# Optimization experiments

Measured on AMD Instinct MI355X. Metric: run time of the kernel, lower is better.

Reference implementation:

```python
import jax, jax.numpy as jnp
import numpy as np

B, S, D, E, H, K = 2, 2048, 1024, 8, 4096, 2


def setup_inputs() -> dict:
    key = jax.random.key(0)
    ks = jax.random.split(key, 8)
    w = lambda i, shape: jax.random.normal(ks[i], shape, jnp.float32) * 0.02
    return {
        "x": jax.random.normal(ks[0], (B, S, D), jnp.float32),
        "noise": jax.random.normal(ks[1], (B, S, E), jnp.float32),
        "Wg": w(2, (E, D)),
        "noise_weight": jnp.zeros((E,), jnp.float32),
        "W1": w(3, (E, D, H)),
        "b1": jnp.zeros((E, H), jnp.float32),
        "W2": w(4, (E, D, H)),
        "b2": jnp.zeros((E, H), jnp.float32),
        "Wp": w(5, (E, H, D)),
        "bp": jnp.zeros((E, D), jnp.float32),
        "k": K,
    }


def reference(x, noise, Wg, noise_weight, W1, b1, W2, b2, Wp, bp, k):
    Bb, Ss, Dd = x.shape
    Ee = Wg.shape[0]
    # --- noisy top-k gate (noisy_std = 1.0) ---
    logits = jnp.einsum('bsd,ed->bse', x, Wg)
    noisy = logits + noise * noise_weight            # [B,S,E]
    vals, idx = jax.lax.top_k(noisy, k)              # [B,S,k]
    oh = jax.nn.one_hot(idx, Ee, dtype=x.dtype)      # [B,S,k,E]
    sel = oh.sum(axis=-2) > 0                        # [B,S,E] selected mask
    scat = (oh * vals[..., None]).sum(axis=-2)       # scatter topk logits
    sparse = jnp.where(sel, scat, -jnp.inf)
    gate = jax.nn.softmax(sparse, axis=-1)           # zero weight off-topk
    # --- dense-equivalent expert compute (gate==0 off top-k => same math as masked dispatch) ---
    xf = x.reshape(Bb * Ss, Dd)                      # [T,D]
    gf = gate.reshape(Bb * Ss, Ee)                   # [T,E]
    h1 = jnp.einsum('td,edh->eth', xf, W1) + b1[:, None, :]
    h2 = jnp.einsum('td,edh->eth', xf, W2) + b2[:, None, :]
    hh = h1 * jax.nn.silu(h2)                        # SwiGLU
    outs = jnp.einsum('eth,ehd->etd', hh, Wp) + bp[:, None, :]
    final = jnp.einsum('etd,te->td', outs, gf).reshape(Bb, Ss, Dd)
    return final, idx
```

## Files before the change

kernel.cpp:

```cpp
#include <hip/hip_runtime.h>
#include <math.h>

#define Bc 2
#define Sc 2048
#define Dc 1024
#define Ec 8
#define Hc 4096
#define Tc (Bc*Sc)
#define NSLOT (Tc*2)
#define FINAL_N ((size_t)Tc*Dc)
#define BK 32

typedef float f32x4 __attribute__((ext_vector_type(4)));
typedef __bf16 bf16x8 __attribute__((ext_vector_type(8)));

__device__ __forceinline__ unsigned short f2bf(float f) {
    union { float f; unsigned int u; } v; v.f = f;
    return (unsigned short)((v.u + 0x7fffu + ((v.u >> 16) & 1u)) >> 16);
}

__device__ __forceinline__ void gload16(const unsigned short* g, unsigned short* l) {
    __builtin_amdgcn_global_load_lds(
        (const __attribute__((address_space(1))) unsigned int*)g,
        (__attribute__((address_space(3))) unsigned int*)l,
        16, 0, 0);
}

__device__ __forceinline__ void fence_bar() {
    __builtin_amdgcn_sched_barrier(0);
    asm volatile("s_barrier" ::: "memory");
    __builtin_amdgcn_sched_barrier(0);
}

__global__ void k_cvt_x(const float* __restrict__ x, unsigned short* __restrict__ xbf) {
    int gid = blockIdx.x * 256 + threadIdx.x;
    const float4* p = (const float4*)x + (size_t)gid * 2;
    float4 a = p[0], b = p[1];
    ushort4 r0 = { f2bf(a.x), f2bf(a.y), f2bf(a.z), f2bf(a.w) };
    ushort4 r1 = { f2bf(b.x), f2bf(b.y), f2bf(b.z), f2bf(b.w) };
    ushort4* o = (ushort4*)xbf + (size_t)gid * 2;
    o[0] = r0; o[1] = r1;
}

__global__ void k_transpose_cvt2(const float* __restrict__ inA, const float* __restrict__ inB,
                                 unsigned short* __restrict__ outA, unsigned short* __restrict__ outB,
                                 int R, int C, int nz_per_mat) {
    __shared__ float tile[64][65];
    int z = blockIdx.z;
    const float* in; unsigned short* out;
    if (z < nz_per_mat) { in = inA; out = outA; }
    else { in = inB; out = outB; z -= nz_per_mat; }
    size_t base = (size_t)z * (size_t)R * C;
    int cb = blockIdx.x * 64, rb = blockIdx.y * 64;
    int t = threadIdx.x;
    int q = t & 15, g = t >> 4;
    #pragma unroll
    for (int j = 0; j < 4; j++) {
        int row = g + 16*j;
        float4 v = *(const float4*)&in[base + (size_t)(rb+row)*C + cb + q*4];
        tile[row][q*4+0] = v.x; tile[row][q*4+1] = v.y;
        tile[row][q*4+2] = v.z; tile[row][q*4+3] = v.w;
    }
    __syncthreads();
    #pragma unroll
    for (int j = 0; j < 4; j++) {
        int co = g + 16*j;
        ushort4 o;
        o.x = f2bf(tile[q*4+0][co]); o.y = f2bf(tile[q*4+1][co]);
        o.z = f2bf(tile[q*4+2][co]); o.w = f2bf(tile[q*4+3][co]);
        *(ushort4*)&out[base + (size_t)(cb+co)*R + rb + q*4] = o;
    }
}

__global__ void k_gate(const float* __restrict__ x, const float* __restrict__ noise,
                       const float* __restrict__ Wg, const float* __restrict__ nw,
                       float* __restrict__ out_idx, int* __restrict__ counts,
                       int* __restrict__ tok_top, float* __restrict__ tok_w) {
    int t = blockIdx.x;
    int lane = threadIdx.x;
    const float* xr = x + (size_t)t * Dc;
    double acc[Ec];
    #pragma unroll
    for (int e = 0; e < Ec; e++) acc[e] = 0.0;
    for (int i = 0; i < Dc/64; i++) {
        int d = lane + i*64;
        double xv = (double)xr[d];
        #pragma unroll
        for (int e = 0; e < Ec; e++) acc[e] += xv * (double)Wg[e*Dc + d];
    }
    #pragma unroll
    for (int e = 0; e < Ec; e++)
        for (int off = 32; off > 0; off >>= 1)
            acc[e] += __shfl_down(acc[e], off);
    if (lane == 0) {
        double noisy[Ec];
        #pragma unroll
        for (int e = 0; e < Ec; e++)
            noisy[e] = acc[e] + (double)noise[t*Ec + e] * (double)nw[e];
        int i0 = 0;
        for (int e = 1; e < Ec; e++) if (noisy[e] > noisy[i0]) i0 = e;
        int i1 = -1;
        for (int e = 0; e < Ec; e++) {
            if (e == i0) continue;
            if (i1 < 0 || noisy[e] > noisy[i1]) i1 = e;
        }
        double ee = exp(noisy[i1] - noisy[i0]);
        float w0 = (float)(1.0 / (1.0 + ee));
        float w1 = (float)(ee / (1.0 + ee));
        out_idx[t*2 + 0] = (float)i0;
        out_idx[t*2 + 1] = (float)i1;
        tok_top[t*2] = i0; tok_top[t*2+1] = i1;
        tok_w[t*2] = w0;   tok_w[t*2+1] = w1;
        atomicAdd(&counts[i0], 1);
        atomicAdd(&counts[i1], 1);
    }
}

__global__ void k_scan(const int* __restrict__ counts, int* __restrict__ offsets) {
    if (threadIdx.x == 0) {
        int s = 0;
        for (int e = 0; e < Ec; e++) { offsets[e] = s; s += counts[e]; }
        offsets[Ec] = s;
    }
}

__global__ void k_fill(const int* __restrict__ tok_top, const int* __restrict__ offsets,
                       int* __restrict__ fill, int* __restrict__ slot_token,
                       int* __restrict__ slot_of) {
    int t = blockIdx.x * 256 + threadIdx.x;
    if (t >= Tc) return;
    #pragma unroll
    for (int j = 0; j < 2; j++) {
        int e = tok_top[t*2 + j];
        int pos = atomicAdd(&fill[e], 1);
        int slot = offsets[e] + pos;
        slot_token[slot] = t;
        slot_of[t*2 + j] = slot;
    }
}

#define BM1 256
#define BN1 128
#define A1SZ (BM1*BK)
#define W1SZ (BN1*BK)

__global__ __launch_bounds__(512, 2) void k_gemm1(
    const unsigned short* __restrict__ xbf,
    const unsigned short* __restrict__ w1t, const unsigned short* __restrict__ w2t,
    const float* __restrict__ b1, const float* __restrict__ b2,
    const int* __restrict__ counts, const int* __restrict__ offsets,
    const int* __restrict__ slot_token,
    unsigned short* __restrict__ hh) {
    int e = blockIdx.z;
    int n_e = counts[e];
    int m0 = blockIdx.y * BM1;
    if (m0 >= n_e) return;
    int base = offsets[e];
    int n0 = blockIdx.x * BN1;

    __shared__ __align__(16) unsigned short sA[3*A1SZ];
    __shared__ __align__(16) unsigned short sW1[3*W1SZ];
    __shared__ __align__(16) unsigned short sW2[3*W1SZ];
    __shared__ int tlist[BM1];

    int tid = threadIdx.x;
    if (tid < BM1) {
        int r = m0 + tid; if (r > n_e - 1) r = n_e - 1;
        tlist[tid] = slot_token[base + r];
    }
    __syncthreads();

    int wid = tid >> 6, lane = tid & 63;
    int wr = wid >> 1, wc = wid & 1;

    int rl = lane >> 2, sc_ = lane & 3;
    int rA0 = wid*32 + rl, rA1 = rA0 + 16;
    int rB  = wid*16 + rl;
    int cA0 = sc_ ^ ((rA0 >> 1) & 3);
    int cA1 = sc_ ^ ((rA1 >> 1) & 3);
    int cB  = sc_ ^ ((rB  >> 1) & 3);
    int tA0 = tlist[rA0], tA1 = tlist[rA1];
    const unsigned short* pa0 = xbf + (size_t)tA0*Dc + cA0*8;
    const unsigned short* pa1 = xbf + (size_t)tA1*Dc + cA1*8;
    const size_t wb = ((size_t)e * Hc + n0) * Dc;
    const unsigned short* pw1 = w1t + wb + (size_t)rB*Dc + cB*8;
    const unsigned short* pw2 = w2t + wb + (size_t)rB*Dc + cB*8;
    int aofs = wid*1024, bofs = wid*512;

    f32x4 acc1[4][4], acc2[4][4];
    #pragma unroll
    for (int m = 0; m < 4; m++)
        #pragma unroll
        for (int n = 0; n < 4; n++)
            #pragma unroll
            for (int j = 0; j < 4; j++) { acc1[m][n][j] = 0.0f; acc2[m][n][j] = 0.0f; }

    int arow = lane & 15, cr = lane >> 4;
    int ccf = cr ^ ((arow >> 1) & 3);
    int offA[4], offW[4];
    #pragma unroll
    for (int m = 0; m < 4; m++) offA[m] = (wr*64 + m*16 + arow)*BK + ccf*8;
    #pragma unroll
    for (int n = 0; n < 4; n++) offW[n] = (wc*64 + n*16 + arow)*BK + ccf*8;

    auto STAGE = [&](int buf, int kk) {
        unsigned short* dA = sA + buf*A1SZ + aofs;
        gload16(pa0 + kk, dA);
        gload16(pa1 + kk, dA + 512);
        gload16(pw1 + kk, sW1 + buf*W1SZ + bofs);
        gload16(pw2 + kk, sW2 + buf*W1SZ + bofs);
    };

#define LDF1(buf, a, w1f, w2f) { \
    const unsigned short* lA_ = sA  + (buf)*A1SZ; \
    const unsigned short* l1_ = sW1 + (buf)*W1SZ; \
    const unsigned short* l2_ = sW2 + (buf)*W1SZ; \
    _Pragma("unroll") for (int m_ = 0; m_ < 4; m_++) a[m_] = *(const bf16x8*)&lA_[offA[m_]]; \
    _Pragma("unroll") for (int n_ = 0; n_ < 4; n_++) { \
        w1f[n_] = *(const bf16x8*)&l1_[offW[n_]]; \
        w2f[n_] = *(const bf16x8*)&l2_[offW[n_]]; } }

#define MM1(a, w1f, w2f) { \
    _Pragma("unroll") for (int m_ = 0; m_ < 4; m_++) \
        _Pragma("unroll") for (int n_ = 0; n_ < 4; n_++) { \
            acc1[m_][n_] = __builtin_amdgcn_mfma_f32_16x16x32_bf16(a[m_], w1f[n_], acc1[m_][n_], 0, 0, 0); \
            acc2[m_][n_] = __builtin_amdgcn_mfma_f32_16x16x32_bf16(a[m_], w2f[n_], acc2[m_][n_], 0, 0, 0); } }

    bf16x8 a0[4], x10[4], x20[4], a1[4], x11[4], x21[4];

    STAGE(0, 0); STAGE(1, BK);
    asm volatile("s_waitcnt vmcnt(4)" ::: "memory");
    fence_bar();
    LDF1(0, a0, x10, x20);
    asm volatile("s_waitcnt lgkmcnt(0)" ::: "memory");
    __builtin_amdgcn_sched_barrier(0);

    const int NT = Dc / BK;
    int ib = 0;

#define G1ITER(T, CA, CW1, CW2, NA, NW1, NW2) { \
    int i1_ = ib + 1; if (i1_ == 3) i1_ = 0; \
    int i2_ = i1_ + 1; if (i2_ == 3) i2_ = 0; \
    if ((T) + 2 < NT) { \
        STAGE(i2_, ((T)+2)*BK); \
        asm volatile("s_waitcnt vmcnt(4)" ::: "memory");    \
    } else if ((T) + 1 < NT) { \
        asm volatile("s_waitcnt vmcnt(0)" ::: "memory"); \
    } \
    fence_bar();                                 \
    __builtin_amdgcn_s_setprio(1); \
    if ((T) + 1 < NT) LDF1(i1_, NA, NW1, NW2);   \
    MM1(CA, CW1, CW2); \
    __builtin_amdgcn_s_setprio(0); \
    asm volatile("s_waitcnt lgkmcnt(0)" ::: "memory"); \
    __builtin_amdgcn_sched_barrier(0); \
    ib = i1_; }

    for (int t = 0; t < NT; t += 2) {
        G1ITER(t,   a0, x10, x20, a1, x11, x21);
        G1ITER(t+1, a1, x11, x21, a0, x10, x20);
    }

    int lrow = (lane >> 4) * 4, lcol = lane & 15;
    #pragma unroll
    for (int n = 0; n < 4; n++) {
        int hcol = n0 + wc*64 + n*16 + lcol;
        float bias1 = b1[e*Hc + hcol], bias2 = b2[e*Hc + hcol];
        #pragma unroll
        for (int m = 0; m < 4; m++) {
            int rb2 = m0 + wr*64 + m*16 + lrow;
            #pragma unroll
            for (int j = 0; j < 4; j++) {
                int r = rb2 + j;
                if (r < n_e) {
                    float h1v = acc1[m][n][j] + bias1;
                    float h2v = acc2[m][n][j] + bias2;
                    float hhv = h1v * (h2v / (1.0f + expf(-h2v)));
                    hh[(size_t)(base + r)*Hc + hcol] = f2bf(hhv);
                }
            }
        }
    }
#undef G1ITER
#undef MM1
#undef LDF1
}

#define BM2 256
#define BN2 128
#define A2SZ (BM2*BK)
#define B2SZ (BN2*BK)

__global__ __launch_bounds__(512, 2) void k_gemm2(
    const unsigned short* __restrict__ hh,
    const unsigned short* __restrict__ wpt,
    const float* __restrict__ bp,
    const int* __restrict__ counts, const int* __restrict__ offsets,
    float* __restrict__ outb) {
    int e = blockIdx.z;
    int n_e = counts[e];
    int m0 = blockIdx.y * BM2;
    if (m0 >= n_e) return;
    int base = offsets[e];
    int n0 = blockIdx.x * BN2;

    __shared__ __align__(16) unsigned short sA[3*A2SZ];
    __shared__ __align__(16) unsigned short sB[3*B2SZ];

    int tid = threadIdx.x;
    int wid = tid >> 6, lane = tid & 63;
    int wr = wid >> 1, wc = wid & 1;

    int rl = lane >> 2, sc_ = lane & 3;
    int rA0 = wid*32 + rl, rA1 = rA0 + 16;
    int rB  = wid*16 + rl;
    int cA0 = sc_ ^ ((rA0 >> 1) & 3);
    int cA1 = sc_ ^ ((rA1 >> 1) & 3);
    int cB  = sc_ ^ ((rB  >> 1) & 3);
    int gr0 = m0 + rA0; if (gr0 > n_e - 1) gr0 = n_e - 1;
    int gr1 = m0 + rA1; if (gr1 > n_e - 1) gr1 = n_e - 1;
    const unsigned short* pa0 = hh + (size_t)(base + gr0)*Hc + cA0*8;
    const unsigned short* pa1 = hh + (size_t)(base + gr1)*Hc + cA1*8;
    const unsigned short* pb  = wpt + ((size_t)e*Dc + n0 + rB)*Hc + cB*8;
    int aofs = wid*1024, bofs = wid*512;

    f32x4 acc[4][4];
    #pragma unroll
    for (int m = 0; m < 4; m++)
        #pragma unroll
        for (int n = 0; n < 4; n++)
            #pragma unroll
            for (int j = 0; j < 4; j++) acc[m][n][j] = 0.0f;

    int arow = lane & 15, cr = lane >> 4;
    int ccf = cr ^ ((arow >> 1) & 3);
    int offA[4], offW[4];
    #pragma unroll
    for (int m = 0; m < 4; m++) offA[m] = (wr*64 + m*16 + arow)*BK + ccf*8;
    #pragma unroll
    for (int n = 0; n < 4; n++) offW[n] = (wc*64 + n*16 + arow)*BK + ccf*8;

    auto STAGE = [&](int buf, int kk) {
        unsigned short* dA = sA + buf*A2SZ + aofs;
        gload16(pa0 + kk, dA);
        gload16(pa1 + kk, dA + 512);
        gload16(pb  + kk, sB + buf*B2SZ + bofs);
    };

#define LDF2(buf, a, b) { \
    const unsigned short* lA_ = sA + (buf)*A2SZ; \
    const unsigned short* lB_ = sB + (buf)*B2SZ; \
    _Pragma("unroll") for (int m_ = 0; m_ < 4; m_++) a[m_] = *(const bf16x8*)&lA_[offA[m_]]; \
    _Pragma("unroll") for (int n_ = 0; n_ < 4; n_++) b[n_] = *(const bf16x8*)&lB_[offW[n_]]; }

#define MM2(a, b) { \
    _Pragma("unroll") for (int m_ = 0; m_ < 4; m_++) \
        _Pragma("unroll") for (int n_ = 0; n_ < 4; n_++) \
            acc[m_][n_] = __builtin_amdgcn_mfma_f32_16x16x32_bf16(a[m_], b[n_], acc[m_][n_], 0, 0, 0); }

    bf16x8 a0[4], b0[4], a1[4], b1f[4];

    STAGE(0, 0); STAGE(1, BK);
    asm volatile("s_waitcnt vmcnt(3)" ::: "memory");
    fence_bar();
    LDF2(0, a0, b0);
    asm volatile("s_waitcnt lgkmcnt(0)" ::: "memory");
    __builtin_amdgcn_sched_barrier(0);

    const int NT = Hc / BK;
    int ib = 0;

#define G2ITER(T, CA, CB, NA, NB) { \
    int i1_ = ib + 1; if (i1_ == 3) i1_ = 0; \
    int i2_ = i1_ + 1; if (i2_ == 3) i2_ = 0; \
    if ((T) + 2 < NT) { \
        STAGE(i2_, ((T)+2)*BK); \
        asm volatile("s_waitcnt vmcnt(3)" ::: "memory"); \
    } else if ((T) + 1 < NT) { \
        asm volatile("s_waitcnt vmcnt(0)" ::: "memory"); \
    } \
    fence_bar(); \
    __builtin_amdgcn_s_setprio(1); \
    if ((T) + 1 < NT) LDF2(i1_, NA, NB); \
    MM2(CA, CB); \
    __builtin_amdgcn_s_setprio(0); \
    asm volatile("s_waitcnt lgkmcnt(0)" ::: "memory"); \
    __builtin_amdgcn_sched_barrier(0); \
    ib = i1_; }

    for (int t = 0; t < NT; t += 2) {
        G2ITER(t,   a0, b0, a1, b1f);
        G2ITER(t+1, a1, b1f, a0, b0);
    }

    int lrow = (lane >> 4) * 4, lcol = lane & 15;
    #pragma unroll
    for (int n = 0; n < 4; n++) {
        int dcol = n0 + wc*64 + n*16 + lcol;
        float bias = bp[e*Dc + dcol];
        #pragma unroll
        for (int m = 0; m < 4; m++) {
            int rb2 = m0 + wr*64 + m*16 + lrow;
            #pragma unroll
            for (int j = 0; j < 4; j++) {
                int r = rb2 + j;
                if (r < n_e)
                    outb[(size_t)(base + r)*Dc + dcol] = acc[m][n][j] + bias;
            }
        }
    }
#undef G2ITER
#undef MM2
#undef LDF2
}

__global__ void k_combine(const float* __restrict__ outb, const int* __restrict__ slot_of,
                          const float* __restrict__ tok_w, float* __restrict__ final_out) {
    int gid = blockIdx.x * 256 + threadIdx.x;
    int t = gid >> 8;
    int c = (gid & 255) * 4;
    int s0 = slot_of[t*2], s1 = slot_of[t*2 + 1];
    float w0 = tok_w[t*2], w1 = tok_w[t*2 + 1];
    float4 o0 = *(const float4*)&outb[(size_t)s0*Dc + c];
    float4 o1 = *(const float4*)&outb[(size_t)s1*Dc + c];
    float4 r;
    r.x = w0*o0.x + w1*o1.x;
    r.y = w0*o0.y + w1*o1.y;
    r.z = w0*o0.z + w1*o1.z;
    r.w = w0*o0.w + w1*o1.w;
    *(float4*)&final_out[(size_t)t*Dc + c] = r;
}

extern "C" void kernel_launch(void* const* d_in, const int* in_sizes, int n_in,
                              void* d_out, int out_size, void* d_ws, size_t ws_size,
                              hipStream_t stream) {
    (void)in_sizes; (void)n_in; (void)out_size; (void)ws_size;
    const float* x     = (const float*)d_in[0];
    const float* noise = (const float*)d_in[1];
    const float* Wg    = (const float*)d_in[2];
    const float* nw    = (const float*)d_in[3];
    const float* W1    = (const float*)d_in[4];
    const float* b1    = (const float*)d_in[5];
    const float* W2    = (const float*)d_in[6];
    const float* b2    = (const float*)d_in[7];
    const float* Wp    = (const float*)d_in[8];
    const float* bp    = (const float*)d_in[9];

    char* ws = (char*)d_ws;
    size_t off = 0;
    unsigned short* XBF = (unsigned short*)(ws + off); off += (size_t)Tc*Dc*2;
    unsigned short* W1T = (unsigned short*)(ws + off); off += (size_t)Ec*Dc*Hc*2;
    unsigned short* W2T = (unsigned short*)(ws + off); off += (size_t)Ec*Dc*Hc*2;
    unsigned short* WPT = (unsigned short*)(ws + off); off += (size_t)Ec*Hc*Dc*2;
    unsigned short* HH  = (unsigned short*)(ws + off); off += (size_t)NSLOT*Hc*2;
    float*          OUTB= (float*)(ws + off);          off += (size_t)NSLOT*Dc*4;
    int*   counts    = (int*)(ws + off);
    int*   fill      = (int*)(ws + off + 32);
    int*   offsets   = (int*)(ws + off + 64);
    int*   tok_top   = (int*)(ws + off + 128);
    float* tok_w     = (float*)(ws + off + 128 + (size_t)Tc*2*4);
    int*   slot_token= (int*)(ws + off + 128 + (size_t)Tc*2*8);
    int*   slot_of   = (int*)(ws + off + 128 + (size_t)Tc*2*8 + (size_t)NSLOT*4);

    float* final_out = (float*)d_out;
    float* idx_out   = (float*)d_out + FINAL_N;

    hipMemsetAsync(counts, 0, 64, stream);

    k_cvt_x<<<(Tc*Dc/8)/256, 256, 0, stream>>>(x, XBF);
    k_transpose_cvt2<<<dim3(Hc/64, Dc/64, 2*Ec), 256, 0, stream>>>(W1, W2, W1T, W2T, Dc, Hc, Ec);
    k_transpose_cvt2<<<dim3(Dc/64, Hc/64, Ec), 256, 0, stream>>>(Wp, Wp, WPT, WPT, Hc, Dc, Ec);

    k_gate<<<Tc, 64, 0, stream>>>(x, noise, Wg, nw, idx_out, counts, tok_top, tok_w);
    k_scan<<<1, 64, 0, stream>>>(counts, offsets);
    k_fill<<<Tc/256, 256, 0, stream>>>(tok_top, offsets, fill, slot_token, slot_of);

    k_gemm1<<<dim3(Hc/BN1, Tc/BM1, Ec), 512, 0, stream>>>(XBF, W1T, W2T, b1, b2,
                                                          counts, offsets, slot_token, HH);
    k_gemm2<<<dim3(Dc/BN2, Tc/BM2, Ec), 512, 0, stream>>>(HH, WPT, bp, counts, offsets, OUTB);
    k_combine<<<(Tc*Dc/4)/256, 256, 0, stream>>>(OUTB, slot_of, tok_w, final_out);
}
```

Measured before the change: 703.1 us.

## Pack GEMM operands into pre-swizzled K-panel layouts for contiguous tile loads

Weights are transposed into 128x32 K-panels with the LDS swizzle already applied. Routed tokens are gathered into a slot-ordered, panel-packed bf16 A matrix by a new pack kernel, and the SwiGLU output is written in the same panel layout. Each wave's global-to-LDS loads then read contiguous 1KB chunks instead of strided rows, which should improve memory coalescing and remove the token-list indirection from GEMM1. The cost is an extra gather/pack kernel, a scattered write pattern in the GEMM1 epilogue, and a more complex indexing scheme that is harder to verify.

After: 696.9 us. No clear change (-0.9%).

```diff
diff --git a/kernel.cpp b/kernel.cpp
--- a/kernel.cpp
+++ b/kernel.cpp
@@ -8,8 +8,10 @@
 #define Hc 4096
 #define Tc (Bc*Sc)
 #define NSLOT (Tc*2)
+#define SLOTPAD 8448
 #define FINAL_N ((size_t)Tc*Dc)
 #define BK 32
+#define PROWS ((size_t)SLOTPAD*32)
 
 typedef float f32x4 __attribute__((ext_vector_type(4)));
 typedef __bf16 bf16x8 __attribute__((ext_vector_type(8)));
@@ -17,6 +19,9 @@
 __device__ __forceinline__ unsigned short f2bf(float f) {
     union { float f; unsigned int u; } v; v.f = f;
     return (unsigned short)((v.u + 0x7fffu + ((v.u >> 16) & 1u)) >> 16);
+}
+__device__ __forceinline__ unsigned int pack2bf(float a, float b) {
+    return (unsigned int)f2bf(a) | ((unsigned int)f2bf(b) << 16);
 }
 
 __device__ __forceinline__ void gload16(const unsigned short* g, unsigned short* l) {
@@ -32,32 +37,23 @@
     __builtin_amdgcn_sched_barrier(0);
 }
 
-__global__ void k_cvt_x(const float* __restrict__ x, unsigned short* __restrict__ xbf) {
-    int gid = blockIdx.x * 256 + threadIdx.x;
-    const float4* p = (const float4*)x + (size_t)gid * 2;
-    float4 a = p[0], b = p[1];
-    ushort4 r0 = { f2bf(a.x), f2bf(a.y), f2bf(a.z), f2bf(a.w) };
-    ushort4 r1 = { f2bf(b.x), f2bf(b.y), f2bf(b.z), f2bf(b.w) };
-    ushort4* o = (ushort4*)xbf + (size_t)gid * 2;
-    o[0] = r0; o[1] = r1;
-}
-
-__global__ void k_transpose_cvt2(const float* __restrict__ inA, const float* __restrict__ inB,
-                                 unsigned short* __restrict__ outA, unsigned short* __restrict__ outB,
-                                 int R, int C, int nz_per_mat) {
+__global__ void k_transpose_panel(const float* __restrict__ inA, const float* __restrict__ inB,
+                                  unsigned short* __restrict__ outA, unsigned short* __restrict__ outB,
+                                  int R, int C, int nz_per_mat) {
     __shared__ float tile[64][65];
     int z = blockIdx.z;
     const float* in; unsigned short* out;
     if (z < nz_per_mat) { in = inA; out = outA; }
     else { in = inB; out = outB; z -= nz_per_mat; }
-    size_t base = (size_t)z * (size_t)R * C;
+    size_t zbase = (size_t)z * (size_t)R * C;
+    int R32 = R >> 5;
     int cb = blockIdx.x * 64, rb = blockIdx.y * 64;
     int t = threadIdx.x;
     int q = t & 15, g = t >> 4;
     #pragma unroll
     for (int j = 0; j < 4; j++) {
         int row = g + 16*j;
-        float4 v = *(const float4*)&in[base + (size_t)(rb+row)*C + cb + q*4];
+        float4 v = *(const float4*)&in[zbase + (size_t)(rb+row)*C + cb + q*4];
         tile[row][q*4+0] = v.x; tile[row][q*4+1] = v.y;
         tile[row][q*4+2] = v.z; tile[row][q*4+3] = v.w;
     }
@@ -65,10 +61,16 @@
     #pragma unroll
     for (int j = 0; j < 4; j++) {
         int co = g + 16*j;
+        int c = cb + co;
+        int r0 = rb + q*4;
         ushort4 o;
         o.x = f2bf(tile[q*4+0][co]); o.y = f2bf(tile[q*4+1][co]);
         o.z = f2bf(tile[q*4+2][co]); o.w = f2bf(tile[q*4+3][co]);
-        *(ushort4*)&out[base + (size_t)(cb+co)*R + rb + q*4] = o;
+        int cr = c & 127;
+        int ch = ((r0 >> 3) & 3) ^ ((cr >> 1) & 3);
+        size_t off = zbase + (((size_t)(c >> 7) * R32 + (r0 >> 5)) * 4096)
+                   + (size_t)cr * 32 + ch * 8 + (r0 & 7);
+        *(ushort4*)&out[off] = o;
     }
 }
 
@@ -126,7 +128,7 @@
 
 __global__ void k_fill(const int* __restrict__ tok_top, const int* __restrict__ offsets,
                        int* __restrict__ fill, int* __restrict__ slot_token,
-                       int* __restrict__ slot_of) {
+                       int* __restrict__ slot_of, int* __restrict__ slot_pos) {
     int t = blockIdx.x * 256 + threadIdx.x;
     if (t >= Tc) return;
     #pragma unroll
@@ -136,7 +138,29 @@
         int slot = offsets[e] + pos;
         slot_token[slot] = t;
         slot_of[t*2 + j] = slot;
-    }
+        slot_pos[slot] = pos;
+    }
+}
+
+__global__ void k_packA(const float* __restrict__ x, const int* __restrict__ slot_token,
+                        const int* __restrict__ slot_pos, unsigned short* __restrict__ apk) {
+    int s = blockIdx.x * 4 + (threadIdx.x >> 6);
+    int lane = threadIdx.x & 63;
+    int token = slot_token[s];
+    int pos = slot_pos[s];
+    const float4* px = (const float4*)(x + (size_t)token * Dc) + lane*4;
+    float4 v0 = px[0], v1 = px[1], v2 = px[2], v3 = px[3];
+    uint4 lo, hi;
+    lo.x = pack2bf(v0.x, v0.y); lo.y = pack2bf(v0.z, v0.w);
+    lo.z = pack2bf(v1.x, v1.y); lo.w = pack2bf(v1.z, v1.w);
+    hi.x = pack2bf(v2.x, v2.y); hi.y = pack2bf(v2.z, v2.w);
+    hi.z = pack2bf(v3.x, v3.y); hi.w = pack2bf(v3.z, v3.w);
+    int kp = lane >> 1;
+    int key = (pos >> 1) & 3;
+    int c0 = (lane & 1) * 2;
+    size_t base = (size_t)kp * PROWS + (size_t)s * 32;
+    *(uint4*)&apk[base + ((c0 ^ key) * 8)]       = lo;
+    *(uint4*)&apk[base + (((c0+1) ^ key) * 8)]   = hi;
 }
 
 #define BM1 256
@@ -145,47 +169,30 @@
 #define W1SZ (BN1*BK)
 
 __global__ __launch_bounds__(512, 2) void k_gemm1(
-    const unsigned short* __restrict__ xbf,
-    const unsigned short* __restrict__ w1t, const unsigned short* __restrict__ w2t,
+    const unsigned short* __restrict__ apk,
+    const unsigned short* __restrict__ w1p, const unsigned short* __restrict__ w2p,
     const float* __restrict__ b1, const float* __restrict__ b2,
     const int* __restrict__ counts, const int* __restrict__ offsets,
-    const int* __restrict__ slot_token,
-    unsigned short* __restrict__ hh) {
+    unsigned short* __restrict__ hh2) {
     int e = blockIdx.z;
     int n_e = counts[e];
     int m0 = blockIdx.y * BM1;
     if (m0 >= n_e) return;
     int base = offsets[e];
-    int n0 = blockIdx.x * BN1;
+    int hp = blockIdx.x;
+    int n0 = hp * BN1;
 
     __shared__ __align__(16) unsigned short sA[3*A1SZ];
     __shared__ __align__(16) unsigned short sW1[3*W1SZ];
     __shared__ __align__(16) unsigned short sW2[3*W1SZ];
-    __shared__ int tlist[BM1];
 
     int tid = threadIdx.x;
-    if (tid < BM1) {
-        int r = m0 + tid; if (r > n_e - 1) r = n_e - 1;
-        tlist[tid] = slot_token[base + r];
-    }
-    __syncthreads();
-
     int wid = tid >> 6, lane = tid & 63;
     int wr = wid >> 1, wc = wid & 1;
 
-    int rl = lane >> 2, sc_ = lane & 3;
-    int rA0 = wid*32 + rl, rA1 = rA0 + 16;
-    int rB  = wid*16 + rl;
-    int cA0 = sc_ ^ ((rA0 >> 1) & 3);
-    int cA1 = sc_ ^ ((rA1 >> 1) & 3);
-    int cB  = sc_ ^ ((rB  >> 1) & 3);
-    int tA0 = tlist[rA0], tA1 = tlist[rA1];
-    const unsigned short* pa0 = xbf + (size_t)tA0*Dc + cA0*8;
-    const unsigned short* pa1 = xbf + (size_t)tA1*Dc + cA1*8;
-    const size_t wb = ((size_t)e * Hc + n0) * Dc;
-    const unsigned short* pw1 = w1t + wb + (size_t)rB*Dc + cB*8;
-    const unsigned short* pw2 = w2t + wb + (size_t)rB*Dc + cB*8;
-    int aofs = wid*1024, bofs = wid*512;
+    const unsigned short* pa  = apk + (size_t)(base + m0 + wid*32) * 32 + lane*8;
+    const unsigned short* pw1 = w1p + ((size_t)(e*32 + hp) * 32) * 4096 + wid*512 + lane*8;
+    const unsigned short* pw2 = w2p + ((size_t)(e*32 + hp) * 32) * 4096 + wid*512 + lane*8;
 
     f32x4 acc1[4][4], acc2[4][4];
     #pragma unroll
@@ -203,12 +210,13 @@
     #pragma unroll
     for (int n = 0; n < 4; n++) offW[n] = (wc*64 + n*16 + arow)*BK + ccf*8;
 
-    auto STAGE = [&](int buf, int kk) {
-        unsigned short* dA = sA + buf*A1SZ + aofs;
-        gload16(pa0 + kk, dA);
-        gload16(pa1 + kk, dA + 512);
-        gload16(pw1 + kk, sW1 + buf*W1SZ + bofs);
-        gload16(pw2 + kk, sW2 + buf*W1SZ + bofs);
+    auto STAGE = [&](int buf, int kp) {
+        unsigned short* dA = sA + buf*A1SZ + wid*1024;
+        const unsigned short* a = pa + (size_t)kp * PROWS;
+        gload16(a,       dA);
+        gload16(a + 512, dA + 512);
+        gload16(pw1 + kp*4096, sW1 + buf*W1SZ + wid*512);
+        gload16(pw2 + kp*4096, sW2 + buf*W1SZ + wid*512);
     };
 
 #define LDF1(buf, a, w1f, w2f) { \
@@ -228,7 +236,7 @@
 
     bf16x8 a0[4], x10[4], x20[4], a1[4], x11[4], x21[4];
 
-    STAGE(0, 0); STAGE(1, BK);
+    STAGE(0, 0); STAGE(1, 1);
     asm volatile("s_waitcnt vmcnt(4)" ::: "memory");
     fence_bar();
     LDF1(0, a0, x10, x20);
@@ -242,7 +250,7 @@
     int i1_ = ib + 1; if (i1_ == 3) i1_ = 0; \
     int i2_ = i1_ + 1; if (i2_ == 3) i2_ = 0; \
     if ((T) + 2 < NT) { \
-        STAGE(i2_, ((T)+2)*BK); \
+        STAGE(i2_, (T)+2); \
         asm volatile("s_waitcnt vmcnt(4)" ::: "memory");    \
     } else if ((T) + 1 < NT) { \
         asm volatile("s_waitcnt vmcnt(0)" ::: "memory"); \
@@ -266,6 +274,9 @@
     for (int n = 0; n < 4; n++) {
         int hcol = n0 + wc*64 + n*16 + lcol;
         float bias1 = b1[e*Hc + hcol], bias2 = b2[e*Hc + hcol];
+        int hp2 = hcol >> 5;
+        int ch  = (hcol >> 3) & 3;
+        int ho  = hcol & 7;
         #pragma unroll
         for (int m = 0; m < 4; m++) {
             int rb2 = m0 + wr*64 + m*16 + lrow;
@@ -276,7 +287,8 @@
                     float h1v = acc1[m][n][j] + bias1;
                     float h2v = acc2[m][n][j] + bias2;
                     float hhv = h1v * (h2v / (1.0f + expf(-h2v)));
-                    hh[(size_t)(base + r)*Hc + hcol] = f2bf(hhv);
+                    int key = (r >> 1) & 3;
+                    hh2[(size_t)hp2 * PROWS + (size_t)(base + r)*32 + ((ch ^ key)*8) + ho] = f2bf(hhv);
                 }
             }
         }
@@ -292,8 +304,8 @@
 #define B2SZ (BN2*BK)
 
 __global__ __launch_bounds__(512, 2) void k_gemm2(
-    const unsigned short* __restrict__ hh,
-    const unsigned short* __restrict__ wpt,
+    const unsigned short* __restrict__ hh2,
+    const unsigned short* __restrict__ wpp,
     const float* __restrict__ bp,
     const int* __restrict__ counts, const int* __restrict__ offsets,
     float* __restrict__ outb) {
@@ -302,7 +314,8 @@
     int m0 = blockIdx.y * BM2;
     if (m0 >= n_e) return;
     int base = offsets[e];
-    int n0 = blockIdx.x * BN2;
+    int dp = blockIdx.x;
+    int n0 = dp * BN2;
 
     __shared__ __align__(16) unsigned short sA[3*A2SZ];
     __shared__ __align__(16) unsigned short sB[3*B2SZ];
@@ -311,18 +324,8 @@
     int wid = tid >> 6, lane = tid & 63;
     int wr = wid >> 1, wc = wid & 1;
 
-    int rl = lane >> 2, sc_ = lane & 3;
-    int rA0 = wid*32 + rl, rA1 = rA0 + 16;
-    int rB  = wid*16 + rl;
-    int cA0 = sc_ ^ ((rA0 >> 1) & 3);
-    int cA1 = sc_ ^ ((rA1 >> 1) & 3);
-    int cB  = sc_ ^ ((rB  >> 1) & 3);
-    int gr0 = m0 + rA0; if (gr0 > n_e - 1) gr0 = n_e - 1;
-    int gr1 = m0 + rA1; if (gr1 > n_e - 1) gr1 = n_e - 1;
-    const unsigned short* pa0 = hh + (size_t)(base + gr0)*Hc + cA0*8;
-    const unsigned short* pa1 = hh + (size_t)(base + gr1)*Hc + cA1*8;
-    const unsigned short* pb  = wpt + ((size_t)e*Dc + n0 + rB)*Hc + cB*8;
-    int aofs = wid*1024, bofs = wid*512;
+    const unsigned short* pa = hh2 + (size_t)(base + m0 + wid*32) * 32 + lane*8;
+    const unsigned short* pb = wpp + ((size_t)(e*8 + dp) * 128) * 4096 + wid*512 + lane*8;
 
     f32x4 acc[4][4];
     #pragma unroll
@@ -340,11 +343,12 @@
     #pragma unroll
     for (int n = 0; n < 4; n++) offW[n] = (wc*64 + n*16 + arow)*BK + ccf*8;
 
-    auto STAGE = [&](int buf, int kk) {
-        unsigned short* dA = sA + buf*A2SZ + aofs;
-        gload16(pa0 + kk, dA);
-        gload16(pa1 + kk, dA + 512);
-        gload16(pb  + kk, sB + buf*B2SZ + bofs);
+    auto STAGE = [&](int buf, int kp) {
+        unsigned short* dA = sA + buf*A2SZ + wid*1024;
+        const unsigned short* a = pa + (size_t)kp * PROWS;
+        gload16(a,       dA);
+        gload16(a + 512, dA + 512);
+        gload16(pb + kp*4096, sB + buf*B2SZ + wid*512);
     };
 
 #define LDF2(buf, a, b) { \
@@ -360,7 +364,7 @@
 
     bf16x8 a0[4], b0[4], a1[4], b1f[4];
 
-    STAGE(0, 0); STAGE(1, BK);
+    STAGE(0, 0); STAGE(1, 1);
     asm volatile("s_waitcnt vmcnt(3)" ::: "memory");
     fence_bar();
     LDF2(0, a0, b0);
@@ -374,7 +378,7 @@
     int i1_ = ib + 1; if (i1_ == 3) i1_ = 0; \
     int i2_ = i1_ + 1; if (i2_ == 3) i2_ = 0; \
     if ((T) + 2 < NT) { \
-        STAGE(i2_, ((T)+2)*BK); \
+        STAGE(i2_, (T)+2); \
         asm volatile("s_waitcnt vmcnt(3)" ::: "memory"); \
     } else if ((T) + 1 < NT) { \
         asm volatile("s_waitcnt vmcnt(0)" ::: "memory"); \
@@ -448,11 +452,11 @@
 
     char* ws = (char*)d_ws;
     size_t off = 0;
-    unsigned short* XBF = (unsigned short*)(ws + off); off += (size_t)Tc*Dc*2;
-    unsigned short* W1T = (unsigned short*)(ws + off); off += (size_t)Ec*Dc*Hc*2;
-    unsigned short* W2T = (unsigned short*)(ws + off); off += (size_t)Ec*Dc*Hc*2;
-    unsigned short* WPT = (unsigned short*)(ws + off); off += (size_t)Ec*Hc*Dc*2;
-    unsigned short* HH  = (unsigned short*)(ws + off); off += (size_t)NSLOT*Hc*2;
+    unsigned short* W1P = (unsigned short*)(ws + off); off += (size_t)Ec*Dc*Hc*2;
+    unsigned short* W2P = (unsigned short*)(ws + off); off += (size_t)Ec*Dc*Hc*2;
+    unsigned short* WPP = (unsigned short*)(ws + off); off += (size_t)Ec*Hc*Dc*2;
+    unsigned short* APK = (unsigned short*)(ws + off); off += (size_t)32*PROWS*2;
+    unsigned short* HH2 = (unsigned short*)(ws + off); off += (size_t)128*PROWS*2;
     float*          OUTB= (float*)(ws + off);          off += (size_t)NSLOT*Dc*4;
     int*   counts    = (int*)(ws + off);
     int*   fill      = (int*)(ws + off + 32);
@@ -461,22 +465,23 @@
     float* tok_w     = (float*)(ws + off + 128 + (size_t)Tc*2*4);
     int*   slot_token= (int*)(ws + off + 128 + (size_t)Tc*2*8);
     int*   slot_of   = (int*)(ws + off + 128 + (size_t)Tc*2*8 + (size_t)NSLOT*4);
+    int*   slot_pos  = (int*)(ws + off + 128 + (size_t)Tc*2*8 + (size_t)NSLOT*8);
 
     float* final_out = (float*)d_out;
     float* idx_out   = (float*)d_out + FINAL_N;
 
     hipMemsetAsync(counts, 0, 64, stream);
 
-    k_cvt_x<<<(Tc*Dc/8)/256, 256, 0, stream>>>(x, XBF);
-    k_transpose_cvt2<<<dim3(Hc/64, Dc/64, 2*Ec), 256, 0, stream>>>(W1, W2, W1T, W2T, Dc, Hc, Ec);
-    k_transpose_cvt2<<<dim3(Dc/64, Hc/64, Ec), 256, 0, stream>>>(Wp, Wp, WPT, WPT, Hc, Dc, Ec);
+    k_transpose_panel<<<dim3(Hc/64, Dc/64, 2*Ec), 256, 0, stream>>>(W1, W2, W1P, W2P, Dc, Hc, Ec);
+    k_transpose_panel<<<dim3(Dc/64, Hc/64, Ec), 256, 0, stream>>>(Wp, Wp, WPP, WPP, Hc, Dc, Ec);
 
     k_gate<<<Tc, 64, 0, stream>>>(x, noise, Wg, nw, idx_out, counts, tok_top, tok_w);
     k_scan<<<1, 64, 0, stream>>>(counts, offsets);
-    k_fill<<<Tc/256, 256, 0, stream>>>(tok_top, offsets, fill, slot_token, slot_of);
-
-    k_gemm1<<<dim3(Hc/BN1, Tc/BM1, Ec), 512, 0, stream>>>(XBF, W1T, W2T, b1, b2,
-                                                          counts, offsets, slot_token, HH);
-    k_gemm2<<<dim3(Dc/BN2, Tc/BM2, Ec), 512, 0, stream>>>(HH, WPT, bp, counts, offsets, OUTB);
+    k_fill<<<Tc/256, 256, 0, stream>>>(tok_top, offsets, fill, slot_token, slot_of, slot_pos);
+    k_packA<<<NSLOT/4, 256, 0, stream>>>(x, slot_token, slot_pos, APK);
+
+    k_gemm1<<<dim3(Hc/BN1, Tc/BM1, Ec), 512, 0, stream>>>(APK, W1P, W2P, b1, b2,
+                                                          counts, offsets, HH2);
+    k_gemm2<<<dim3(Dc/BN2, Tc/BM2, Ec), 512, 0, stream>>>(HH2, WPP, bp, counts, offsets, OUTB);
     k_combine<<<(Tc*Dc/4)/256, 256, 0, stream>>>(OUTB, slot_of, tok_w, final_out);
 }
```
